# Kernel tuning notes

Measured on AMD Instinct MI355X. Metric: run time of the kernel, lower is better.

Reference implementation:

```python
import jax, jax.numpy as jnp
import numpy as np

KERN = 2  # matches init kwarg


def _avgpool(x):
    # non-overlapping avg pool kernel=stride=KERN on (N,C,H,W)
    N, C, H, W = x.shape
    return x.reshape(N, C, H // KERN, KERN, W // KERN, KERN).mean(axis=(3, 5))


def _pair_sum(mu1, var1, mu2, var2):
    # mu*, var*: (N, D). Broadcast to (N, N, D) and reduce to scalar.
    d = mu1[:, None, :] - mu2[None, :, :]
    s = var1[:, None, :] + var2[None, :, :]
    return jnp.sum(jnp.exp(-0.5 * (d * d / s + jnp.log(s))))


def setup_inputs() -> dict:
    key = jax.random.key(0)
    k1, k2, k3, k4 = jax.random.split(key, 4)
    shp = (128, 16, 32, 32)
    return {
        "mu_a": jax.random.normal(k1, shp, dtype=jnp.float32),
        "logvar_a": jax.random.normal(k2, shp, dtype=jnp.float32),
        "mu_b": jax.random.normal(k3, shp, dtype=jnp.float32),
        "logvar_b": jax.random.normal(k4, shp, dtype=jnp.float32),
    }


def reference(mu_a, logvar_a, mu_b, logvar_b):
    inv_k2 = 1.0 / (KERN * KERN)
    ma = _avgpool(mu_a)
    mb = _avgpool(mu_b)
    va = _avgpool(jnp.exp(logvar_a)) * inv_k2
    vb = _avgpool(jnp.exp(logvar_b)) * inv_k2
    N = ma.shape[0]
    ma, mb = ma.reshape(N, -1), mb.reshape(N, -1)
    va, vb = va.reshape(N, -1), vb.reshape(N, -1)
    vaa = _pair_sum(ma, va, ma, va)
    vab = _pair_sum(ma, va, mb, vb)
    vbb = _pair_sum(mb, vb, mb, vb)
    return vaa + vbb - 2.0 * vab
```

## Files before the change

### kernel.cpp

```cpp
#include <hip/hip_runtime.h>

#define NN 128
#define CC_ 16
#define HH 32
#define WW 32
#define DD 4096
#define ND (NN*DD)

typedef float v2f __attribute__((ext_vector_type(2)));

#define MU_SCALE 0.8493218002880191f

__global__ __launch_bounds__(256) void pool_kernel(
    const float* __restrict__ mu_a, const float* __restrict__ lv_a,
    const float* __restrict__ mu_b, const float* __restrict__ lv_b,
    float4* __restrict__ wmv, float* __restrict__ out)
{
    int t = blockIdx.x * 256 + threadIdx.x;
    if (t == 0) out[0] = 0.0f;

    int wo = t & 15;
    int ho = (t >> 4) & 15;
    int c  = (t >> 8) & 15;
    int n  = t >> 12;

    int base = ((n * CC_ + c) * HH + 2 * ho) * WW + 2 * wo;

    float2 a0 = *(const float2*)(mu_a + base);
    float2 a1 = *(const float2*)(mu_a + base + WW);
    float2 la0 = *(const float2*)(lv_a + base);
    float2 la1 = *(const float2*)(lv_a + base + WW);
    float2 b0 = *(const float2*)(mu_b + base);
    float2 b1 = *(const float2*)(mu_b + base + WW);
    float2 lb0 = *(const float2*)(lv_b + base);
    float2 lb1 = *(const float2*)(lv_b + base + WW);

    const float ms = 0.25f * MU_SCALE;
    float ma_v = ms * (a0.x + a0.y + a1.x + a1.y);
    float mb_v = ms * (b0.x + b0.y + b1.x + b1.y);
    float va_v = 0.0625f * (__expf(la0.x) + __expf(la0.y) + __expf(la1.x) + __expf(la1.y));
    float vb_v = 0.0625f * (__expf(lb0.x) + __expf(lb0.y) + __expf(lb1.x) + __expf(lb1.y));

    wmv[t] = make_float4(ma_v, mb_v, va_v, vb_v);
}

__device__ __forceinline__ void pair_group(
    v2f& acc, v2f mi, v2f mj, v2f vi, v2f vj)
{
    v2f dd = mi - mj;
    v2f s  = vi + vj;
    v2f r;
    r.x = __builtin_amdgcn_rsqf(s.x);
    r.y = __builtin_amdgcn_rsqf(s.y);
    v2f q  = dd * r;
    v2f qq = q * q;
    v2f e;
    e.x = __builtin_amdgcn_exp2f(-qq.x);
    e.y = __builtin_amdgcn_exp2f(-qq.y);
    acc += e * r;
}

__device__ __forceinline__ void pair_group_w(
    v2f& acc, v2f w, v2f mi, v2f mj, v2f vi, v2f vj)
{
    v2f dd = mi - mj;
    v2f s  = vi + vj;
    v2f r;
    r.x = __builtin_amdgcn_rsqf(s.x);
    r.y = __builtin_amdgcn_rsqf(s.y);
    v2f q  = dd * r;
    v2f qq = q * q;
    v2f e;
    e.x = __builtin_amdgcn_exp2f(-qq.x);
    e.y = __builtin_amdgcn_exp2f(-qq.y);
    v2f er = e * r;
    acc += w * er;
}

__device__ __forceinline__ void run_range(
    int jlo, int jhi, int i0, int d,
    const float4* __restrict__ wmv,
    v2f& acc_aa, v2f& acc_bb, v2f& acc_ab,
    const v2f pma[2], const v2f pmb[2], const v2f pva[2], const v2f pvb[2])
{
    const int below_end = min(jhi, i0);
    const int band_lo   = max(jlo, i0);
    const int band_hi   = min(jhi, i0 + 4);
    const int above_lo  = max(jlo, i0 + 4);

#pragma unroll 2
    for (int j = jlo; j < below_end; ++j) {
        float4 jr = wmv[j * DD + d];
        v2f jma2 = (v2f){jr.x, jr.x};
        v2f jmb2 = (v2f){jr.y, jr.y};
        v2f jva2 = (v2f){jr.z, jr.z};
        v2f jvb2 = (v2f){jr.w, jr.w};
#pragma unroll
        for (int p = 0; p < 2; ++p) {
            pair_group(acc_aa, pma[p], jma2, pva[p], jva2);
            pair_group(acc_bb, pmb[p], jmb2, pvb[p], jvb2);
            pair_group(acc_ab, pma[p], jmb2, pva[p], jvb2);
        }
    }

    for (int j = band_lo; j < band_hi; ++j) {
        float4 jr = wmv[j * DD + d];
        v2f jma2 = (v2f){jr.x, jr.x};
        v2f jmb2 = (v2f){jr.y, jr.y};
        v2f jva2 = (v2f){jr.z, jr.z};
        v2f jvb2 = (v2f){jr.w, jr.w};
        v2f w[2];
#pragma unroll
        for (int p = 0; p < 2; ++p) {
            int r0 = i0 + 2 * p, r1 = r0 + 1;
            w[p].x = (j < r0) ? 1.0f : (j == r0 ? 0.5f : 0.0f);
            w[p].y = (j < r1) ? 1.0f : (j == r1 ? 0.5f : 0.0f);
        }
#pragma unroll
        for (int p = 0; p < 2; ++p) {
            pair_group_w(acc_aa, w[p], pma[p], jma2, pva[p], jva2);
            pair_group_w(acc_bb, w[p], pmb[p], jmb2, pvb[p], jvb2);
            pair_group(acc_ab, pma[p], jmb2, pva[p], jvb2);
        }
    }

#pragma unroll 2
    for (int j = above_lo; j < jhi; ++j) {
        float4 jr = wmv[j * DD + d];
        v2f jmb2 = (v2f){jr.y, jr.y};
        v2f jvb2 = (v2f){jr.w, jr.w};
#pragma unroll
        for (int p = 0; p < 2; ++p) {
            pair_group(acc_ab, pma[p], jmb2, pva[p], jvb2);
        }
    }
}

__global__ __launch_bounds__(256) void pair_kernel(
    const float4* __restrict__ wmv, float* __restrict__ out)
{
    const int d  = blockIdx.x * 256 + threadIdx.x;
    const int ti = blockIdx.y >> 2;
    const int pp = blockIdx.y & 3;
    const int i0 = ti * 4;
    const int c0 = pp;
    const int c1 = 7 - pp;

    v2f pma[2], pmb[2], pva[2], pvb[2];
#pragma unroll
    for (int p = 0; p < 2; ++p) {
        float4 r0 = wmv[(i0 + 2 * p) * DD + d];
        float4 r1 = wmv[(i0 + 2 * p + 1) * DD + d];
        pma[p] = (v2f){r0.x, r1.x};
        pmb[p] = (v2f){r0.y, r1.y};
        pva[p] = (v2f){r0.z, r1.z};
        pvb[p] = (v2f){r0.w, r1.w};
    }

    v2f acc_aa = (v2f){0.0f, 0.0f};
    v2f acc_bb = (v2f){0.0f, 0.0f};
    v2f acc_ab = (v2f){0.0f, 0.0f};

    run_range(c0 * 16, c0 * 16 + 16, i0, d, wmv,
              acc_aa, acc_bb, acc_ab, pma, pmb, pva, pvb);
    run_range(c1 * 16, c1 * 16 + 16, i0, d, wmv,
              acc_aa, acc_bb, acc_ab, pma, pmb, pva, pvb);

    float part = 2.0f * ((acc_aa.x + acc_aa.y) + (acc_bb.x + acc_bb.y)
                       - (acc_ab.x + acc_ab.y));

#pragma unroll
    for (int off = 32; off > 0; off >>= 1)
        part += __shfl_down(part, off, 64);

    __shared__ float wsum[4];
    int lane = threadIdx.x & 63;
    int wv_  = threadIdx.x >> 6;
    if (lane == 0) wsum[wv_] = part;
    __syncthreads();
    if (threadIdx.x == 0) {
        float s = wsum[0] + wsum[1] + wsum[2] + wsum[3];
        atomicAdd(out, s);
    }
}

extern "C" void kernel_launch(void* const* d_in, const int* in_sizes, int n_in,
                              void* d_out, int out_size, void* d_ws, size_t ws_size,
                              hipStream_t stream) {
    const float* mu_a = (const float*)d_in[0];
    const float* lv_a = (const float*)d_in[1];
    const float* mu_b = (const float*)d_in[2];
    const float* lv_b = (const float*)d_in[3];
    float* out  = (float*)d_out;
    float4* wmv = (float4*)d_ws;

    pool_kernel<<<dim3(ND / 256), 256, 0, stream>>>(mu_a, lv_a, mu_b, lv_b, wmv, out);
    pair_kernel<<<dim3(DD / 256, 128), 256, 0, stream>>>(wmv, out);
}
```

Before: 115.4 us.

## Rebalance pair kernel by pairing heavy below-diagonal units with light above-diagonal units

Replaces the fixed chunk pairing per tile with an explicit mapping. Each block processes two (tile, chunk) units: one heavy unit (chunk below the tile, all three pair terms) and one light unit (chunk above, cross term only). This is meant to equalize per-block work and reduce load imbalance and tail effects. It adds index-decoding branches and a second load of pivot rows per block.

```diff
diff --git a/kernel.cpp b/kernel.cpp
--- a/kernel.cpp
+++ b/kernel.cpp
@@ -136,16 +136,11 @@
     }
 }
 
-__global__ __launch_bounds__(256) void pair_kernel(
-    const float4* __restrict__ wmv, float* __restrict__ out)
-{
-    const int d  = blockIdx.x * 256 + threadIdx.x;
-    const int ti = blockIdx.y >> 2;
-    const int pp = blockIdx.y & 3;
-    const int i0 = ti * 4;
-    const int c0 = pp;
-    const int c1 = 7 - pp;
-
+__device__ __forceinline__ void process_unit(
+    int tile, int chunk, int d, const float4* __restrict__ wmv,
+    v2f& acc_aa, v2f& acc_bb, v2f& acc_ab)
+{
+    const int i0 = tile * 4;
     v2f pma[2], pmb[2], pva[2], pvb[2];
 #pragma unroll
     for (int p = 0; p < 2; ++p) {
@@ -156,15 +151,60 @@
         pva[p] = (v2f){r0.z, r1.z};
         pvb[p] = (v2f){r0.w, r1.w};
     }
+    run_range(chunk * 16, chunk * 16 + 16, i0, d, wmv,
+              acc_aa, acc_bb, acc_ab, pma, pmb, pva, pvb);
+}
+
+__device__ __forceinline__ uint2 heavy_below(int k) {
+    int tile, c;
+    if (k < 16)      { tile = 16 + (k >> 2);            c = k & 3; }
+    else if (k < 36) { int kk = k - 16; tile = 20 + kk / 5; c = kk % 5; }
+    else if (k < 60) { int kk = k - 36; tile = 24 + kk / 6; c = kk % 6; }
+    else             { int kk = k - 60; tile = 28 + kk / 7; c = kk % 7; }
+    return make_uint2(tile, c);
+}
+__device__ __forceinline__ uint2 light_above(int k) {
+    int tile, c;
+    if (k < 28)      { tile = k / 7;                    c = 1 + k % 7; }
+    else if (k < 52) { int kk = k - 28; tile = 4 + kk / 6;  c = 2 + kk % 6; }
+    else if (k < 72) { int kk = k - 52; tile = 8 + kk / 5;  c = 3 + kk % 5; }
+    else             { int kk = k - 72; tile = 12 + (kk >> 2); c = 4 + (kk & 3); }
+    return make_uint2(tile, c);
+}
+__device__ __forceinline__ uint2 light_below(int k) {
+    int tile, c;
+    if (k < 4)       { tile = 4 + k;                    c = 0; }
+    else if (k < 12) { int kk = k - 4;  tile = 8 + (kk >> 1);  c = kk & 1; }
+    else             { int kk = k - 12; tile = 12 + kk / 3; c = kk % 3; }
+    return make_uint2(tile, c);
+}
+__device__ __forceinline__ uint2 heavy_above(int k) {
+    int tile, c;
+    if (k < 12)      { tile = 16 + k / 3;               c = 5 + k % 3; }
+    else if (k < 20) { int kk = k - 12; tile = 20 + (kk >> 1); c = 6 + (kk & 1); }
+    else             { tile = 24 + (k - 20);            c = 7; }
+    return make_uint2(tile, c);
+}
+
+__global__ __launch_bounds__(256) void pair_kernel(
+    const float4* __restrict__ wmv, float* __restrict__ out)
+{
+    const int d = blockIdx.x * 256 + threadIdx.x;
+    const int y = blockIdx.y;
+
+    uint2 A, B;
+    if (y < 88)       { A = heavy_below(y);       B = light_above(y); }
+    else if (y < 112) { A = light_below(y - 88);  B = heavy_above(y - 88); }
+    else              { int k = y - 112;
+                        A = make_uint2(k, k >> 2);
+                        B = make_uint2(31 - k, (31 - k) >> 2); }
 
     v2f acc_aa = (v2f){0.0f, 0.0f};
     v2f acc_bb = (v2f){0.0f, 0.0f};
     v2f acc_ab = (v2f){0.0f, 0.0f};
 
-    run_range(c0 * 16, c0 * 16 + 16, i0, d, wmv,
-              acc_aa, acc_bb, acc_ab, pma, pmb, pva, pvb);
-    run_range(c1 * 16, c1 * 16 + 16, i0, d, wmv,
-              acc_aa, acc_bb, acc_ab, pma, pmb, pva, pvb);
+    process_unit((int)A.x, (int)A.y, d, wmv, acc_aa, acc_bb, acc_ab);
+    process_unit((int)B.x, (int)B.y, d, wmv, acc_aa, acc_bb, acc_ab);
 
     float part = 2.0f * ((acc_aa.x + acc_aa.y) + (acc_bb.x + acc_bb.y)
                        - (acc_ab.x + acc_ab.y));
```

New measurement: 112.5 us, median of 2. -2.5%, faster.
